# Kernel optimization log

Hardware: AMD Instinct MI355X
Metric: run time of the kernel (lower is better)

## Reference

```python
import jax, jax.numpy as jnp
import numpy as np

M_ZEROS = 15
ZETA_WEIGHT = 0.4
SIGMA = 0.1
# First 15 imaginary parts of nontrivial Riemann zeta zeros (get_zeta_zeros(15))
ZETA_ZEROS = np.array([
    14.134725, 21.022040, 25.010858, 30.424876, 32.935062,
    37.586178, 40.918719, 43.327073, 48.005151, 49.773832,
    52.970321, 56.446248, 59.347044, 60.831779, 65.112544,
], dtype=np.float32)

B, T, I, H = 64, 1024, 512, 512


def setup_inputs() -> dict:
    key = jax.random.key(0)
    k = jax.random.split(key, 6)
    s_ih = 1.0 / np.sqrt(I)
    s_hh = 1.0 / np.sqrt(H)
    x = jax.random.normal(k[0], (B, T, I), dtype=jnp.float32)
    W_ih = jax.random.normal(k[1], (4 * H, I), dtype=jnp.float32) * s_ih
    W_hh = jax.random.normal(k[2], (4 * H, H), dtype=jnp.float32) * s_hh
    b_ih = jax.random.normal(k[3], (4 * H,), dtype=jnp.float32) * s_hh
    b_hh = jax.random.normal(k[4], (4 * H,), dtype=jnp.float32) * s_hh
    gammas = jnp.asarray(ZETA_ZEROS)
    phi_init = np.exp(-SIGMA * np.abs(ZETA_ZEROS))
    log_phi = jnp.asarray(np.log(np.exp(phi_init) - 1 + 1e-6).astype(np.float32))
    return {"x": x, "W_ih": W_ih, "W_hh": W_hh, "b_ih": b_ih,
            "b_hh": b_hh, "log_phi": log_phi, "gammas": gammas}


def _zeta_lstm(x, W_ih, W_hh, b_ih, b_hh, log_phi, gammas):
    Bq, Tq, _ = x.shape
    Hq = W_hh.shape[1]
    # Precompute scalar zeta mixing weight per timestep: w_t = sum(phi * cos(g*t)) / M
    phi = jax.nn.softplus(log_phi)                     # [M]
    t_idx = jnp.arange(Tq, dtype=jnp.float32)          # [T]
    cos_mat = jnp.cos(t_idx[:, None] * gammas[None, :])  # [T, M]
    w_ts = (cos_mat @ phi) / M_ZEROS                   # [T]
    # Hoist the input projection out of the scan: [B,T,4H]
    x_proj = jnp.einsum('bti,gi->btg', x, W_ih) + b_ih + b_hh

    def step(carry, inp):
        h, c = carry
        xp_t, w_t = inp
        gates = xp_t + h @ W_hh.T                      # [B, 4H]
        ig, fg, gg, og = jnp.split(gates, 4, axis=-1)
        c_new = jax.nn.sigmoid(fg) * c + jax.nn.sigmoid(ig) * jnp.tanh(gg)
        h_new = jax.nn.sigmoid(og) * jnp.tanh(c_new)
        # zeta memory uses the PREVIOUS h
        h_out = h_new + ZETA_WEIGHT * (w_t * h)
        return (h_out, c_new), h_out

    h0 = jnp.zeros((Bq, Hq), dtype=x.dtype)
    c0 = jnp.zeros((Bq, Hq), dtype=x.dtype)
    xs = (jnp.transpose(x_proj, (1, 0, 2)), w_ts)
    (h_f, c_f), outs = jax.lax.scan(step, (h0, c0), xs)
    outputs = jnp.transpose(outs, (1, 0, 2))           # [B, T, H]
    return outputs, h_f[None, :, :], c_f[None, :, :]


def reference(x, W_ih, W_hh, b_ih, b_hh, log_phi, gammas):
    return _zeta_lstm(x, W_ih, W_hh, b_ih, b_hh, log_phi, gammas)
```

## Files before the change

### kernel.cpp

```cpp
#include <hip/hip_runtime.h>

#define BDIM 64
#define TDIM 1024
#define IDIM 512
#define HDIM 512
#define G4   2048
#define DSLAB 8
#define SLAB_ELEMS (BDIM * HDIM)
#define GROUP_ELEMS (16 * HDIM)

typedef unsigned short u16;
typedef unsigned int u32;
typedef unsigned long long u64;
typedef __attribute__((ext_vector_type(8))) short short8;
typedef __attribute__((ext_vector_type(4))) float f32x4;

__device__ __forceinline__ u16 f2bf(float f) {
    union { float f; unsigned u; } v; v.f = f;
    unsigned u = v.u;
    return (u16)((u + 0x7fffu + ((u >> 16) & 1u)) >> 16);
}
__device__ __forceinline__ float bf2f(u16 h) {
    union { unsigned u; float f; } v; v.u = ((unsigned)h) << 16;
    return v.f;
}
__device__ __forceinline__ float fsig(float x) {
    float e = __builtin_amdgcn_exp2f(x * -1.4426950408889634f);
    return __builtin_amdgcn_rcpf(1.0f + e);
}
__device__ __forceinline__ float ftanh(float x) {
    float e = __builtin_amdgcn_exp2f(x * -2.8853900817779268f);
    return 2.0f * __builtin_amdgcn_rcpf(1.0f + e) - 1.0f;
}

__global__ void prep_kernel(const float* __restrict__ Whh,
                            const float* __restrict__ bih,
                            const float* __restrict__ bhh,
                            const float* __restrict__ log_phi,
                            const float* __restrict__ gammas,
                            u16* __restrict__ whh_bf,
                            float* __restrict__ bias,
                            float* __restrict__ wfull,
                            u32* __restrict__ hbuf32) {
    int idx = blockIdx.x * 256 + threadIdx.x;
    if (idx < G4 * HDIM) whh_bf[idx] = f2bf(Whh[idx]);
    if (idx < G4) bias[idx] = bih[idx] + bhh[idx];
    if (idx < DSLAB * (SLAB_ELEMS / 2))
        hbuf32[idx] = (idx < (SLAB_ELEMS / 2)) ? 0u : 0xffffffffu;
    if (idx < TDIM) {
        float acc = 0.0f;
        #pragma unroll
        for (int m = 0; m < 15; ++m) {
            float lp = log_phi[m];
            float sp = (lp > 15.0f) ? lp : log1pf(expf(lp));
            acc += sp * cosf((float)idx * gammas[m]);
        }
        wfull[idx] = 0.4f * acc / 15.0f;
    }
}

__global__ __launch_bounds__(256) void xproj_gemm(
        const float* __restrict__ X, const float* __restrict__ Wih,
        const float* __restrict__ bias, u16* __restrict__ xproj) {
    const int tid  = threadIdx.x;
    const int m0   = blockIdx.x * 128;
    const int n0   = blockIdx.y * 128;
    const int lane = tid & 63, w = tid >> 6;
    const int l16  = lane & 15, lhi = lane >> 4;
    const int wr   = w >> 1, wc = w & 1;

    __shared__ u16 As[128 * 64];
    __shared__ u16 Bs[128 * 64];

    f32x4 acc[4][4];
    #pragma unroll
    for (int i = 0; i < 4; ++i)
        #pragma unroll
        for (int j = 0; j < 4; ++j) acc[i][j] = (f32x4){0.f, 0.f, 0.f, 0.f};

    for (int kt = 0; kt < 8; ++kt) {
        const int k0 = kt * 64;
        __syncthreads();
        #pragma unroll
        for (int p = 0; p < 4; ++p) {
            int g = p * 256 + tid;
            int row = g >> 3, oct = g & 7;
            const float* src = X + (size_t)(m0 + row) * IDIM + k0 + oct * 8;
            float4 v0 = *(const float4*)src;
            float4 v1 = *(const float4*)(src + 4);
            short8 u;
            u[0] = (short)f2bf(v0.x); u[1] = (short)f2bf(v0.y);
            u[2] = (short)f2bf(v0.z); u[3] = (short)f2bf(v0.w);
            u[4] = (short)f2bf(v1.x); u[5] = (short)f2bf(v1.y);
            u[6] = (short)f2bf(v1.z); u[7] = (short)f2bf(v1.w);
            int so = (oct ^ (row & 7)) * 8;
            *(short8*)&As[row * 64 + so] = u;
        }
        #pragma unroll
        for (int p = 0; p < 4; ++p) {
            int g = p * 256 + tid;
            int row = g >> 3, oct = g & 7;
            const float* src = Wih + (size_t)(n0 + row) * IDIM + k0 + oct * 8;
            float4 v0 = *(const float4*)src;
            float4 v1 = *(const float4*)(src + 4);
            short8 u;
            u[0] = (short)f2bf(v0.x); u[1] = (short)f2bf(v0.y);
            u[2] = (short)f2bf(v0.z); u[3] = (short)f2bf(v0.w);
            u[4] = (short)f2bf(v1.x); u[5] = (short)f2bf(v1.y);
            u[6] = (short)f2bf(v1.z); u[7] = (short)f2bf(v1.w);
            int so = (oct ^ (row & 7)) * 8;
            *(short8*)&Bs[row * 64 + so] = u;
        }
        __syncthreads();
        #pragma unroll
        for (int ks = 0; ks < 2; ++ks) {
            short8 a[4], b[4];
            #pragma unroll
            for (int ai = 0; ai < 4; ++ai) {
                int row = 64 * wr + 16 * ai + l16;
                int oct = (4 * ks + lhi) ^ (row & 7);
                a[ai] = *(const short8*)&As[row * 64 + oct * 8];
            }
            #pragma unroll
            for (int bi = 0; bi < 4; ++bi) {
                int row = 64 * wc + 16 * bi + l16;
                int oct = (4 * ks + lhi) ^ (row & 7);
                b[bi] = *(const short8*)&Bs[row * 64 + oct * 8];
            }
            #pragma unroll
            for (int ai = 0; ai < 4; ++ai)
                #pragma unroll
                for (int bi = 0; bi < 4; ++bi)
                    acc[ai][bi] = __builtin_amdgcn_mfma_f32_16x16x32_bf16(
                        a[ai], b[bi], acc[ai][bi], 0, 0, 0);
        }
    }
    float bv[4];
    #pragma unroll
    for (int bi = 0; bi < 4; ++bi) bv[bi] = bias[n0 + 64 * wc + 16 * bi + l16];
    #pragma unroll
    for (int ai = 0; ai < 4; ++ai) {
        int grow_base = m0 + 64 * wr + 16 * ai + 4 * lhi;
        #pragma unroll
        for (int bi = 0; bi < 4; ++bi) {
            int gcol = n0 + 64 * wc + 16 * bi + l16;
            #pragma unroll
            for (int r = 0; r < 4; ++r) {
                int grow = grow_base + r;
                int b = grow >> 10;
                int t = grow & 1023;
                xproj[((size_t)t * BDIM + b) * G4 + gcol] =
                    f2bf(acc[ai][bi][r] + bv[bi]);
            }
        }
    }
}

__global__ __launch_bounds__(256, 1) void scan_kernel(
        const u16* __restrict__ whh_bf, const float* __restrict__ wfull,
        const u16* __restrict__ xproj, u16* __restrict__ hbuf,
        float* __restrict__ out) {
    const int tid = threadIdx.x;
    const int blk = blockIdx.x;
    const int bg  = blk >> 4;
    const int cgp = blk & 15;
    const int b0  = bg * 16;
    const int c0  = cgp * 32;
    const int lane = tid & 63, w = tid >> 6;
    const int l16 = lane & 15, lhi = lane >> 4;

    __shared__ u16  hfrag[16 * 64 * 8];
    __shared__ float gates[16 * 128];
    __shared__ float wt_s[TDIM];

    for (int i = tid; i < TDIM; i += 256) wt_s[i] = wfull[i];

    short8 Bf0[16], Bf1[16];
    #pragma unroll
    for (int ks = 0; ks < 16; ++ks) {
        int row0 = w * HDIM + c0 + l16;
        int row1 = w * HDIM + c0 + 16 + l16;
        Bf0[ks] = *(const short8*)&whh_bf[(size_t)row0 * HDIM + ks * 32 + lhi * 8];
        Bf1[ks] = *(const short8*)&whh_bf[(size_t)row1 * HDIM + ks * 32 + lhi * 8];
    }

    const int eb = tid >> 4;
    const int j0 = 2 * (tid & 15);
    const int gcol = c0 + j0;
    const int ln_e = eb + 16 * (j0 >> 3);
    const size_t eidx = ((size_t)cgp * 64 + ln_e) * 8 + (j0 & 7);
    float creg0 = 0.f, creg1 = 0.f;
    float hp0 = 0.f, hp1 = 0.f;

    u32 xq0, xq1, xq2, xq3;
    {
        const u16* xb = xproj + (size_t)(b0 + eb) * G4 + gcol;
        xq0 = *(const u32*)(xb + 0 * HDIM);
        xq1 = *(const u32*)(xb + 1 * HDIM);
        xq2 = *(const u32*)(xb + 2 * HDIM);
        xq3 = *(const u32*)(xb + 3 * HDIM);
    }
    __syncthreads();

    for (int t = 0; t < TDIM; ++t) {
        const u16* hsrc = hbuf + (size_t)(t & 7) * SLAB_ELEMS
                               + (size_t)bg * GROUP_ELEMS;

        union F { u64 q[2]; short8 s; } A4[4];
        for (;;) {
            u32 bad = 0;
            #pragma unroll
            for (int i = 0; i < 4; ++i) {
                const int ks = 4 * w + i;
                const u64* p = (const u64*)(hsrc + ks * 512 + lane * 8);
                u64 lo = __hip_atomic_load(p, __ATOMIC_RELAXED, __HIP_MEMORY_SCOPE_AGENT);
                u64 hi = __hip_atomic_load(p + 1, __ATOMIC_RELAXED, __HIP_MEMORY_SCOPE_AGENT);
                A4[i].q[0] = lo; A4[i].q[1] = hi;
                bad |= ((u32)lo == 0xffffffffu) | ((u32)(lo >> 32) == 0xffffffffu) |
                       ((u32)hi == 0xffffffffu) | ((u32)(hi >> 32) == 0xffffffffu);
            }
            if (!__any((int)bad)) break;
        }

        if (t > 0) {
            *(float2*)(out + ((size_t)(b0 + eb) * TDIM + (t - 1)) * HDIM + gcol) =
                make_float2(hp0, hp1);
        }
        u32 nx0 = 0, nx1 = 0, nx2 = 0, nx3 = 0;
        if (t + 1 < TDIM) {
            const u16* xb = xproj + (size_t)(t + 1) * BDIM * G4 +
                            (size_t)(b0 + eb) * G4 + gcol;
            nx0 = *(const u32*)(xb + 0 * HDIM);
            nx1 = *(const u32*)(xb + 1 * HDIM);
            nx2 = *(const u32*)(xb + 2 * HDIM);
            nx3 = *(const u32*)(xb + 3 * HDIM);
        }

        #pragma unroll
        for (int i = 0; i < 4; ++i) {
            const int ks = 4 * w + i;
            *(short8*)&hfrag[(ks * 64 + lane) * 8] = A4[i].s;
        }
        __syncthreads();
        if (t > 0) {
            __hip_atomic_store(
                (u32*)(hbuf + (size_t)((t - 1) & 7) * SLAB_ELEMS +
                       (size_t)bg * GROUP_ELEMS + eidx), 0xffffffffu,
                __ATOMIC_RELAXED, __HIP_MEMORY_SCOPE_AGENT);
        }

        f32x4 acc0a = {0.f, 0.f, 0.f, 0.f}, acc0b = {0.f, 0.f, 0.f, 0.f};
        f32x4 acc1a = {0.f, 0.f, 0.f, 0.f}, acc1b = {0.f, 0.f, 0.f, 0.f};
        #pragma unroll
        for (int ks = 0; ks < 8; ++ks) {
            short8 a  = *(const short8*)&hfrag[(ks * 64 + lane) * 8];
            short8 a2 = *(const short8*)&hfrag[((ks + 8) * 64 + lane) * 8];
            acc0a = __builtin_amdgcn_mfma_f32_16x16x32_bf16(a,  Bf0[ks],     acc0a, 0, 0, 0);
            acc1a = __builtin_amdgcn_mfma_f32_16x16x32_bf16(a,  Bf1[ks],     acc1a, 0, 0, 0);
            acc0b = __builtin_amdgcn_mfma_f32_16x16x32_bf16(a2, Bf0[ks + 8], acc0b, 0, 0, 0);
            acc1b = __builtin_amdgcn_mfma_f32_16x16x32_bf16(a2, Bf1[ks + 8], acc1b, 0, 0, 0);
        }
        f32x4 acc0 = acc0a + acc0b;
        f32x4 acc1 = acc1a + acc1b;
        #pragma unroll
        for (int r = 0; r < 4; ++r) {
            gates[(4 * lhi + r) * 128 + w * 32 + l16]      = acc0[r];
            gates[(4 * lhi + r) * 128 + w * 32 + 16 + l16] = acc1[r];
        }
        __syncthreads();

        const float wt = wt_s[t];
        float x0 = bf2f((u16)(xq0 & 0xffff)), x1 = bf2f((u16)(xq0 >> 16));
        float f0 = bf2f((u16)(xq1 & 0xffff)), f1 = bf2f((u16)(xq1 >> 16));
        float g0 = bf2f((u16)(xq2 & 0xffff)), g1 = bf2f((u16)(xq2 >> 16));
        float o0 = bf2f((u16)(xq3 & 0xffff)), o1 = bf2f((u16)(xq3 >> 16));

        float gi0 = gates[eb * 128 + 0 * 32 + j0]     + x0;
        float gi1 = gates[eb * 128 + 0 * 32 + j0 + 1] + x1;
        float gf0 = gates[eb * 128 + 1 * 32 + j0]     + f0;
        float gf1 = gates[eb * 128 + 1 * 32 + j0 + 1] + f1;
        float gg0 = gates[eb * 128 + 2 * 32 + j0]     + g0;
        float gg1 = gates[eb * 128 + 2 * 32 + j0 + 1] + g1;
        float go0 = gates[eb * 128 + 3 * 32 + j0]     + o0;
        float go1 = gates[eb * 128 + 3 * 32 + j0 + 1] + o1;

        float cn0 = fsig(gf0) * creg0 + fsig(gi0) * ftanh(gg0);
        float cn1 = fsig(gf1) * creg1 + fsig(gi1) * ftanh(gg1);
        float ho0 = fsig(go0) * ftanh(cn0) + wt * hp0;
        float ho1 = fsig(go1) * ftanh(cn1) + wt * hp1;
        creg0 = cn0; creg1 = cn1;
        hp0 = ho0; hp1 = ho1;

        u32 hw = (u32)f2bf(ho0) | ((u32)f2bf(ho1) << 16);
        __hip_atomic_store(
            (u32*)(hbuf + (size_t)((t + 1) & 7) * SLAB_ELEMS +
                   (size_t)bg * GROUP_ELEMS + eidx), hw,
            __ATOMIC_RELAXED, __HIP_MEMORY_SCOPE_AGENT);

        xq0 = nx0; xq1 = nx1; xq2 = nx2; xq3 = nx3;
    }

    *(float2*)(out + ((size_t)(b0 + eb) * TDIM + (TDIM - 1)) * HDIM + gcol) =
        make_float2(hp0, hp1);
    size_t base = (size_t)BDIM * TDIM * HDIM;
    *(float2*)(out + base + (size_t)(b0 + eb) * HDIM + gcol) =
        make_float2(hp0, hp1);
    *(float2*)(out + base + (size_t)BDIM * HDIM + (size_t)(b0 + eb) * HDIM + gcol) =
        make_float2(creg0, creg1);
}

extern "C" void kernel_launch(void* const* d_in, const int* in_sizes, int n_in,
                              void* d_out, int out_size, void* d_ws, size_t ws_size,
                              hipStream_t stream) {
    const float* x       = (const float*)d_in[0];
    const float* Wih     = (const float*)d_in[1];
    const float* Whh     = (const float*)d_in[2];
    const float* bih     = (const float*)d_in[3];
    const float* bhh     = (const float*)d_in[4];
    const float* log_phi = (const float*)d_in[5];
    const float* gammas  = (const float*)d_in[6];
    float* out = (float*)d_out;

    char* ws = (char*)d_ws;
    u16*   whh_bf = (u16*)(ws);
    float* bias   = (float*)(ws + (2u << 20));
    float* wfull  = (float*)(ws + (2u << 20) + 8192);
    u16*   hbuf   = (u16*)(ws + (3u << 20));
    u16*   xproj  = (u16*)(ws + (4u << 20));

    prep_kernel<<<dim3(4096), dim3(256), 0, stream>>>(
        Whh, bih, bhh, log_phi, gammas, whh_bf, bias, wfull, (u32*)hbuf);

    xproj_gemm<<<dim3(512, 16), dim3(256), 0, stream>>>(x, Wih, bias, xproj);

    scan_kernel<<<dim3(64), dim3(256), 0, stream>>>(
        whh_bf, wfull, xproj, hbuf, out);
}
```

Baseline: 2.673 ms.

## Fuse input-projection GEMM with recurrent scan using poisoned xproj flags

Merges the input-projection GEMM and the sequential LSTM scan into one launch. The first 64 blocks run the scan while the remaining blocks compute xproj tiles ordered by time chunk. The scan spins on per-element 0xffff poison values, written into xproj by the prep kernel, until the data it needs is ready. This is meant to overlap the GEMM with the latency-bound recurrence, at the cost of a 256 MB poison fill in prep, atomic loads on xproj, and a deadlock risk if scan blocks occupy CUs before producer blocks are scheduled. A real bf16 value of 0xffff (a NaN pattern) would also spin forever.

```diff
diff --git a/kernel.cpp b/kernel.cpp
--- a/kernel.cpp
+++ b/kernel.cpp
@@ -8,12 +8,14 @@
 #define DSLAB 8
 #define SLAB_ELEMS (BDIM * HDIM)
 #define GROUP_ELEMS (16 * HDIM)
+#define XPROJ_U32 ((size_t)BDIM * TDIM * G4 / 2)
 
 typedef unsigned short u16;
 typedef unsigned int u32;
 typedef unsigned long long u64;
 typedef __attribute__((ext_vector_type(8))) short short8;
 typedef __attribute__((ext_vector_type(4))) float f32x4;
+typedef __attribute__((ext_vector_type(4))) unsigned int u32x4;
 
 __device__ __forceinline__ u16 f2bf(float f) {
     union { float f; unsigned u; } v; v.f = f;
@@ -31,6 +33,9 @@
 __device__ __forceinline__ float ftanh(float x) {
     float e = __builtin_amdgcn_exp2f(x * -2.8853900817779268f);
     return 2.0f * __builtin_amdgcn_rcpf(1.0f + e) - 1.0f;
+}
+__device__ __forceinline__ u32 pois(u32 w) {
+    return ((w & 0xffffu) == 0xffffu) | ((w >> 16) == 0xffffu);
 }
 
 __global__ void prep_kernel(const float* __restrict__ Whh,
@@ -41,9 +46,10 @@
                             u16* __restrict__ whh_bf,
                             float* __restrict__ bias,
                             float* __restrict__ wfull,
-                            u32* __restrict__ hbuf32) {
-    int idx = blockIdx.x * 256 + threadIdx.x;
-    if (idx < G4 * HDIM) whh_bf[idx] = f2bf(Whh[idx]);
+                            u32* __restrict__ hbuf32,
+                            u32* __restrict__ xproj32) {
+    size_t idx = (size_t)blockIdx.x * 256 + threadIdx.x;
+    if (idx < (size_t)G4 * HDIM) whh_bf[idx] = f2bf(Whh[idx]);
     if (idx < G4) bias[idx] = bih[idx] + bhh[idx];
     if (idx < DSLAB * (SLAB_ELEMS / 2))
         hbuf32[idx] = (idx < (SLAB_ELEMS / 2)) ? 0u : 0xffffffffu;
@@ -57,256 +63,273 @@
         }
         wfull[idx] = 0.4f * acc / 15.0f;
     }
-}
-
-__global__ __launch_bounds__(256) void xproj_gemm(
+    if (idx < XPROJ_U32 / 4) {
+        u32x4 p = {0xffffffffu, 0xffffffffu, 0xffffffffu, 0xffffffffu};
+        *(u32x4*)(xproj32 + idx * 4) = p;
+    }
+}
+
+__global__ __launch_bounds__(256, 1) void fused_kernel(
+        const u16* __restrict__ whh_bf, const float* __restrict__ wfull,
         const float* __restrict__ X, const float* __restrict__ Wih,
-        const float* __restrict__ bias, u16* __restrict__ xproj) {
-    const int tid  = threadIdx.x;
-    const int m0   = blockIdx.x * 128;
-    const int n0   = blockIdx.y * 128;
-    const int lane = tid & 63, w = tid >> 6;
-    const int l16  = lane & 15, lhi = lane >> 4;
-    const int wr   = w >> 1, wc = w & 1;
-
-    __shared__ u16 As[128 * 64];
-    __shared__ u16 Bs[128 * 64];
-
-    f32x4 acc[4][4];
-    #pragma unroll
-    for (int i = 0; i < 4; ++i)
-        #pragma unroll
-        for (int j = 0; j < 4; ++j) acc[i][j] = (f32x4){0.f, 0.f, 0.f, 0.f};
-
-    for (int kt = 0; kt < 8; ++kt) {
-        const int k0 = kt * 64;
-        __syncthreads();
-        #pragma unroll
-        for (int p = 0; p < 4; ++p) {
-            int g = p * 256 + tid;
-            int row = g >> 3, oct = g & 7;
-            const float* src = X + (size_t)(m0 + row) * IDIM + k0 + oct * 8;
-            float4 v0 = *(const float4*)src;
-            float4 v1 = *(const float4*)(src + 4);
-            short8 u;
-            u[0] = (short)f2bf(v0.x); u[1] = (short)f2bf(v0.y);
-            u[2] = (short)f2bf(v0.z); u[3] = (short)f2bf(v0.w);
-            u[4] = (short)f2bf(v1.x); u[5] = (short)f2bf(v1.y);
-            u[6] = (short)f2bf(v1.z); u[7] = (short)f2bf(v1.w);
-            int so = (oct ^ (row & 7)) * 8;
-            *(short8*)&As[row * 64 + so] = u;
-        }
-        #pragma unroll
-        for (int p = 0; p < 4; ++p) {
-            int g = p * 256 + tid;
-            int row = g >> 3, oct = g & 7;
-            const float* src = Wih + (size_t)(n0 + row) * IDIM + k0 + oct * 8;
-            float4 v0 = *(const float4*)src;
-            float4 v1 = *(const float4*)(src + 4);
-            short8 u;
-            u[0] = (short)f2bf(v0.x); u[1] = (short)f2bf(v0.y);
-            u[2] = (short)f2bf(v0.z); u[3] = (short)f2bf(v0.w);
-            u[4] = (short)f2bf(v1.x); u[5] = (short)f2bf(v1.y);
-            u[6] = (short)f2bf(v1.z); u[7] = (short)f2bf(v1.w);
-            int so = (oct ^ (row & 7)) * 8;
-            *(short8*)&Bs[row * 64 + so] = u;
-        }
-        __syncthreads();
-        #pragma unroll
-        for (int ks = 0; ks < 2; ++ks) {
-            short8 a[4], b[4];
-            #pragma unroll
-            for (int ai = 0; ai < 4; ++ai) {
-                int row = 64 * wr + 16 * ai + l16;
-                int oct = (4 * ks + lhi) ^ (row & 7);
-                a[ai] = *(const short8*)&As[row * 64 + oct * 8];
-            }
-            #pragma unroll
-            for (int bi = 0; bi < 4; ++bi) {
-                int row = 64 * wc + 16 * bi + l16;
-                int oct = (4 * ks + lhi) ^ (row & 7);
-                b[bi] = *(const short8*)&Bs[row * 64 + oct * 8];
-            }
-            #pragma unroll
-            for (int ai = 0; ai < 4; ++ai)
-                #pragma unroll
-                for (int bi = 0; bi < 4; ++bi)
-                    acc[ai][bi] = __builtin_amdgcn_mfma_f32_16x16x32_bf16(
-                        a[ai], b[bi], acc[ai][bi], 0, 0, 0);
-        }
-    }
-    float bv[4];
-    #pragma unroll
-    for (int bi = 0; bi < 4; ++bi) bv[bi] = bias[n0 + 64 * wc + 16 * bi + l16];
-    #pragma unroll
-    for (int ai = 0; ai < 4; ++ai) {
-        int grow_base = m0 + 64 * wr + 16 * ai + 4 * lhi;
-        #pragma unroll
-        for (int bi = 0; bi < 4; ++bi) {
-            int gcol = n0 + 64 * wc + 16 * bi + l16;
-            #pragma unroll
-            for (int r = 0; r < 4; ++r) {
-                int grow = grow_base + r;
-                int b = grow >> 10;
-                int t = grow & 1023;
-                xproj[((size_t)t * BDIM + b) * G4 + gcol] =
-                    f2bf(acc[ai][bi][r] + bv[bi]);
-            }
-        }
-    }
-}
-
-__global__ __launch_bounds__(256, 1) void scan_kernel(
-        const u16* __restrict__ whh_bf, const float* __restrict__ wfull,
-        const u16* __restrict__ xproj, u16* __restrict__ hbuf,
-        float* __restrict__ out) {
+        const float* __restrict__ bias, u16* __restrict__ xproj,
+        u16* __restrict__ hbuf, float* __restrict__ out) {
     const int tid = threadIdx.x;
-    const int blk = blockIdx.x;
-    const int bg  = blk >> 4;
-    const int cgp = blk & 15;
-    const int b0  = bg * 16;
-    const int c0  = cgp * 32;
     const int lane = tid & 63, w = tid >> 6;
     const int l16 = lane & 15, lhi = lane >> 4;
 
-    __shared__ u16  hfrag[16 * 64 * 8];
-    __shared__ float gates[16 * 128];
-    __shared__ float wt_s[TDIM];
-
-    for (int i = tid; i < TDIM; i += 256) wt_s[i] = wfull[i];
-
-    short8 Bf0[16], Bf1[16];
-    #pragma unroll
-    for (int ks = 0; ks < 16; ++ks) {
-        int row0 = w * HDIM + c0 + l16;
-        int row1 = w * HDIM + c0 + 16 + l16;
-        Bf0[ks] = *(const short8*)&whh_bf[(size_t)row0 * HDIM + ks * 32 + lhi * 8];
-        Bf1[ks] = *(const short8*)&whh_bf[(size_t)row1 * HDIM + ks * 32 + lhi * 8];
-    }
-
-    const int eb = tid >> 4;
-    const int j0 = 2 * (tid & 15);
-    const int gcol = c0 + j0;
-    const int ln_e = eb + 16 * (j0 >> 3);
-    const size_t eidx = ((size_t)cgp * 64 + ln_e) * 8 + (j0 & 7);
-    float creg0 = 0.f, creg1 = 0.f;
-    float hp0 = 0.f, hp1 = 0.f;
-
-    u32 xq0, xq1, xq2, xq3;
-    {
-        const u16* xb = xproj + (size_t)(b0 + eb) * G4 + gcol;
-        xq0 = *(const u32*)(xb + 0 * HDIM);
-        xq1 = *(const u32*)(xb + 1 * HDIM);
-        xq2 = *(const u32*)(xb + 2 * HDIM);
-        xq3 = *(const u32*)(xb + 3 * HDIM);
-    }
-    __syncthreads();
-
-    for (int t = 0; t < TDIM; ++t) {
-        const u16* hsrc = hbuf + (size_t)(t & 7) * SLAB_ELEMS
-                               + (size_t)bg * GROUP_ELEMS;
-
-        union F { u64 q[2]; short8 s; } A4[4];
-        for (;;) {
-            u32 bad = 0;
+    __shared__ char smem[32768];
+
+    if (blockIdx.x < 64) {
+        u16*   hfrag = (u16*)smem;
+        float* gates = (float*)(smem + 16384);
+        float* wt_s  = (float*)(smem + 24576);
+
+        const int blk = blockIdx.x;
+        const int bg  = blk >> 4;
+        const int cgp = blk & 15;
+        const int b0  = bg * 16;
+        const int c0  = cgp * 32;
+
+        for (int i = tid; i < TDIM; i += 256) wt_s[i] = wfull[i];
+
+        short8 Bf0[16], Bf1[16];
+        #pragma unroll
+        for (int ks = 0; ks < 16; ++ks) {
+            int row0 = w * HDIM + c0 + l16;
+            int row1 = w * HDIM + c0 + 16 + l16;
+            Bf0[ks] = *(const short8*)&whh_bf[(size_t)row0 * HDIM + ks * 32 + lhi * 8];
+            Bf1[ks] = *(const short8*)&whh_bf[(size_t)row1 * HDIM + ks * 32 + lhi * 8];
+        }
+
+        const int eb = tid >> 4;
+        const int j0 = 2 * (tid & 15);
+        const int gcol = c0 + j0;
+        const int ln_e = eb + 16 * (j0 >> 3);
+        const size_t eidx = ((size_t)cgp * 64 + ln_e) * 8 + (j0 & 7);
+        float creg0 = 0.f, creg1 = 0.f;
+        float hp0 = 0.f, hp1 = 0.f;
+
+        u32 xq0, xq1, xq2, xq3;
+        {
+            const u16* xb = xproj + (size_t)(b0 + eb) * G4 + gcol;
+            xq0 = __hip_atomic_load((const u32*)(xb + 0 * HDIM), __ATOMIC_RELAXED, __HIP_MEMORY_SCOPE_AGENT);
+            xq1 = __hip_atomic_load((const u32*)(xb + 1 * HDIM), __ATOMIC_RELAXED, __HIP_MEMORY_SCOPE_AGENT);
+            xq2 = __hip_atomic_load((const u32*)(xb + 2 * HDIM), __ATOMIC_RELAXED, __HIP_MEMORY_SCOPE_AGENT);
+            xq3 = __hip_atomic_load((const u32*)(xb + 3 * HDIM), __ATOMIC_RELAXED, __HIP_MEMORY_SCOPE_AGENT);
+        }
+        __syncthreads();
+
+        for (int t = 0; t < TDIM; ++t) {
+            const u16* hsrc = hbuf + (size_t)(t & 7) * SLAB_ELEMS
+                                   + (size_t)bg * GROUP_ELEMS;
+
+            union F { u64 q[2]; short8 s; } A4[4];
+            for (;;) {
+                u32 bad = 0;
+                #pragma unroll
+                for (int i = 0; i < 4; ++i) {
+                    const int ks = 4 * w + i;
+                    const u64* p = (const u64*)(hsrc + ks * 512 + lane * 8);
+                    u64 lo = __hip_atomic_load(p, __ATOMIC_RELAXED, __HIP_MEMORY_SCOPE_AGENT);
+                    u64 hi = __hip_atomic_load(p + 1, __ATOMIC_RELAXED, __HIP_MEMORY_SCOPE_AGENT);
+                    A4[i].q[0] = lo; A4[i].q[1] = hi;
+                    bad |= ((u32)lo == 0xffffffffu) | ((u32)(lo >> 32) == 0xffffffffu) |
+                           ((u32)hi == 0xffffffffu) | ((u32)(hi >> 32) == 0xffffffffu);
+                }
+                if (!__any((int)bad)) break;
+            }
+
+            while (pois(xq0) | pois(xq1) | pois(xq2) | pois(xq3)) {
+                const u16* xb = xproj + (size_t)t * BDIM * G4 +
+                                (size_t)(b0 + eb) * G4 + gcol;
+                xq0 = __hip_atomic_load((const u32*)(xb + 0 * HDIM), __ATOMIC_RELAXED, __HIP_MEMORY_SCOPE_AGENT);
+                xq1 = __hip_atomic_load((const u32*)(xb + 1 * HDIM), __ATOMIC_RELAXED, __HIP_MEMORY_SCOPE_AGENT);
+                xq2 = __hip_atomic_load((const u32*)(xb + 2 * HDIM), __ATOMIC_RELAXED, __HIP_MEMORY_SCOPE_AGENT);
+                xq3 = __hip_atomic_load((const u32*)(xb + 3 * HDIM), __ATOMIC_RELAXED, __HIP_MEMORY_SCOPE_AGENT);
+            }
+
+            if (t > 0) {
+                *(float2*)(out + ((size_t)(b0 + eb) * TDIM + (t - 1)) * HDIM + gcol) =
+                    make_float2(hp0, hp1);
+            }
+            u32 nx0 = 0, nx1 = 0, nx2 = 0, nx3 = 0;
+            if (t + 1 < TDIM) {
+                const u16* xb = xproj + (size_t)(t + 1) * BDIM * G4 +
+                                (size_t)(b0 + eb) * G4 + gcol;
+                nx0 = __hip_atomic_load((const u32*)(xb + 0 * HDIM), __ATOMIC_RELAXED, __HIP_MEMORY_SCOPE_AGENT);
+                nx1 = __hip_atomic_load((const u32*)(xb + 1 * HDIM), __ATOMIC_RELAXED, __HIP_MEMORY_SCOPE_AGENT);
+                nx2 = __hip_atomic_load((const u32*)(xb + 2 * HDIM), __ATOMIC_RELAXED, __HIP_MEMORY_SCOPE_AGENT);
+                nx3 = __hip_atomic_load((const u32*)(xb + 3 * HDIM), __ATOMIC_RELAXED, __HIP_MEMORY_SCOPE_AGENT);
+            }
+
             #pragma unroll
             for (int i = 0; i < 4; ++i) {
                 const int ks = 4 * w + i;
-                const u64* p = (const u64*)(hsrc + ks * 512 + lane * 8);
-                u64 lo = __hip_atomic_load(p, __ATOMIC_RELAXED, __HIP_MEMORY_SCOPE_AGENT);
-                u64 hi = __hip_atomic_load(p + 1, __ATOMIC_RELAXED, __HIP_MEMORY_SCOPE_AGENT);
-                A4[i].q[0] = lo; A4[i].q[1] = hi;
-                bad |= ((u32)lo == 0xffffffffu) | ((u32)(lo >> 32) == 0xffffffffu) |
-                       ((u32)hi == 0xffffffffu) | ((u32)(hi >> 32) == 0xffffffffu);
-            }
-            if (!__any((int)bad)) break;
-        }
-
-        if (t > 0) {
-            *(float2*)(out + ((size_t)(b0 + eb) * TDIM + (t - 1)) * HDIM + gcol) =
-                make_float2(hp0, hp1);
-        }
-        u32 nx0 = 0, nx1 = 0, nx2 = 0, nx3 = 0;
-        if (t + 1 < TDIM) {
-            const u16* xb = xproj + (size_t)(t + 1) * BDIM * G4 +
-                            (size_t)(b0 + eb) * G4 + gcol;
-            nx0 = *(const u32*)(xb + 0 * HDIM);
-            nx1 = *(const u32*)(xb + 1 * HDIM);
-            nx2 = *(const u32*)(xb + 2 * HDIM);
-            nx3 = *(const u32*)(xb + 3 * HDIM);
-        }
-
-        #pragma unroll
-        for (int i = 0; i < 4; ++i) {
-            const int ks = 4 * w + i;
-            *(short8*)&hfrag[(ks * 64 + lane) * 8] = A4[i].s;
-        }
-        __syncthreads();
-        if (t > 0) {
+                *(short8*)&hfrag[(ks * 64 + lane) * 8] = A4[i].s;
+            }
+            __syncthreads();
+            if (t > 0) {
+                __hip_atomic_store(
+                    (u32*)(hbuf + (size_t)((t - 1) & 7) * SLAB_ELEMS +
+                           (size_t)bg * GROUP_ELEMS + eidx), 0xffffffffu,
+                    __ATOMIC_RELAXED, __HIP_MEMORY_SCOPE_AGENT);
+            }
+
+            f32x4 acc0a = {0.f, 0.f, 0.f, 0.f}, acc0b = {0.f, 0.f, 0.f, 0.f};
+            f32x4 acc1a = {0.f, 0.f, 0.f, 0.f}, acc1b = {0.f, 0.f, 0.f, 0.f};
+            #pragma unroll
+            for (int ks = 0; ks < 8; ++ks) {
+                short8 a  = *(const short8*)&hfrag[(ks * 64 + lane) * 8];
+                short8 a2 = *(const short8*)&hfrag[((ks + 8) * 64 + lane) * 8];
+                acc0a = __builtin_amdgcn_mfma_f32_16x16x32_bf16(a,  Bf0[ks],     acc0a, 0, 0, 0);
+                acc1a = __builtin_amdgcn_mfma_f32_16x16x32_bf16(a,  Bf1[ks],     acc1a, 0, 0, 0);
+                acc0b = __builtin_amdgcn_mfma_f32_16x16x32_bf16(a2, Bf0[ks + 8], acc0b, 0, 0, 0);
+                acc1b = __builtin_amdgcn_mfma_f32_16x16x32_bf16(a2, Bf1[ks + 8], acc1b, 0, 0, 0);
+            }
+            f32x4 acc0 = acc0a + acc0b;
+            f32x4 acc1 = acc1a + acc1b;
+            #pragma unroll
+            for (int r = 0; r < 4; ++r) {
+                gates[(4 * lhi + r) * 128 + w * 32 + l16]      = acc0[r];
+                gates[(4 * lhi + r) * 128 + w * 32 + 16 + l16] = acc1[r];
+            }
+            __syncthreads();
+
+            const float wt = wt_s[t];
+            float x0 = bf2f((u16)(xq0 & 0xffff)), x1 = bf2f((u16)(xq0 >> 16));
+            float f0 = bf2f((u16)(xq1 & 0xffff)), f1 = bf2f((u16)(xq1 >> 16));
+            float g0 = bf2f((u16)(xq2 & 0xffff)), g1 = bf2f((u16)(xq2 >> 16));
+            float o0 = bf2f((u16)(xq3 & 0xffff)), o1 = bf2f((u16)(xq3 >> 16));
+
+            float gi0 = gates[eb * 128 + 0 * 32 + j0]     + x0;
+            float gi1 = gates[eb * 128 + 0 * 32 + j0 + 1] + x1;
+            float gf0 = gates[eb * 128 + 1 * 32 + j0]     + f0;
+            float gf1 = gates[eb * 128 + 1 * 32 + j0 + 1] + f1;
+            float gg0 = gates[eb * 128 + 2 * 32 + j0]     + g0;
+            float gg1 = gates[eb * 128 + 2 * 32 + j0 + 1] + g1;
+            float go0 = gates[eb * 128 + 3 * 32 + j0]     + o0;
+            float go1 = gates[eb * 128 + 3 * 32 + j0 + 1] + o1;
+
+            float cn0 = fsig(gf0) * creg0 + fsig(gi0) * ftanh(gg0);
+            float cn1 = fsig(gf1) * creg1 + fsig(gi1) * ftanh(gg1);
+            float ho0 = fsig(go0) * ftanh(cn0) + wt * hp0;
+            float ho1 = fsig(go1) * ftanh(cn1) + wt * hp1;
+            creg0 = cn0; creg1 = cn1;
+            hp0 = ho0; hp1 = ho1;
+
+            u32 hw = (u32)f2bf(ho0) | ((u32)f2bf(ho1) << 16);
             __hip_atomic_store(
-                (u32*)(hbuf + (size_t)((t - 1) & 7) * SLAB_ELEMS +
-                       (size_t)bg * GROUP_ELEMS + eidx), 0xffffffffu,
+                (u32*)(hbuf + (size_t)((t + 1) & 7) * SLAB_ELEMS +
+                       (size_t)bg * GROUP_ELEMS + eidx), hw,
                 __ATOMIC_RELAXED, __HIP_MEMORY_SCOPE_AGENT);
-        }
-
-        f32x4 acc0a = {0.f, 0.f, 0.f, 0.f}, acc0b = {0.f, 0.f, 0.f, 0.f};
-        f32x4 acc1a = {0.f, 0.f, 0.f, 0.f}, acc1b = {0.f, 0.f, 0.f, 0.f};
-        #pragma unroll
-        for (int ks = 0; ks < 8; ++ks) {
-            short8 a  = *(const short8*)&hfrag[(ks * 64 + lane) * 8];
-            short8 a2 = *(const short8*)&hfrag[((ks + 8) * 64 + lane) * 8];
-            acc0a = __builtin_amdgcn_mfma_f32_16x16x32_bf16(a,  Bf0[ks],     acc0a, 0, 0, 0);
-            acc1a = __builtin_amdgcn_mfma_f32_16x16x32_bf16(a,  Bf1[ks],     acc1a, 0, 0, 0);
-            acc0b = __builtin_amdgcn_mfma_f32_16x16x32_bf16(a2, Bf0[ks + 8], acc0b, 0, 0, 0);
-            acc1b = __builtin_amdgcn_mfma_f32_16x16x32_bf16(a2, Bf1[ks + 8], acc1b, 0, 0, 0);
-        }
-        f32x4 acc0 = acc0a + acc0b;
-        f32x4 acc1 = acc1a + acc1b;
-        #pragma unroll
-        for (int r = 0; r < 4; ++r) {
-            gates[(4 * lhi + r) * 128 + w * 32 + l16]      = acc0[r];
-            gates[(4 * lhi + r) * 128 + w * 32 + 16 + l16] = acc1[r];
-        }
-        __syncthreads();
-
-        const float wt = wt_s[t];
-        float x0 = bf2f((u16)(xq0 & 0xffff)), x1 = bf2f((u16)(xq0 >> 16));
-        float f0 = bf2f((u16)(xq1 & 0xffff)), f1 = bf2f((u16)(xq1 >> 16));
-        float g0 = bf2f((u16)(xq2 & 0xffff)), g1 = bf2f((u16)(xq2 >> 16));
-        float o0 = bf2f((u16)(xq3 & 0xffff)), o1 = bf2f((u16)(xq3 >> 16));
-
-        float gi0 = gates[eb * 128 + 0 * 32 + j0]     + x0;
-        float gi1 = gates[eb * 128 + 0 * 32 + j0 + 1] + x1;
-        float gf0 = gates[eb * 128 + 1 * 32 + j0]     + f0;
-        float gf1 = gates[eb * 128 + 1 * 32 + j0 + 1] + f1;
-        float gg0 = gates[eb * 128 + 2 * 32 + j0]     + g0;
-        float gg1 = gates[eb * 128 + 2 * 32 + j0 + 1] + g1;
-        float go0 = gates[eb * 128 + 3 * 32 + j0]     + o0;
-        float go1 = gates[eb * 128 + 3 * 32 + j0 + 1] + o1;
-
-        float cn0 = fsig(gf0) * creg0 + fsig(gi0) * ftanh(gg0);
-        float cn1 = fsig(gf1) * creg1 + fsig(gi1) * ftanh(gg1);
-        float ho0 = fsig(go0) * ftanh(cn0) + wt * hp0;
-        float ho1 = fsig(go1) * ftanh(cn1) + wt * hp1;
-        creg0 = cn0; creg1 = cn1;
-        hp0 = ho0; hp1 = ho1;
-
-        u32 hw = (u32)f2bf(ho0) | ((u32)f2bf(ho1) << 16);
-        __hip_atomic_store(
-            (u32*)(hbuf + (size_t)((t + 1) & 7) * SLAB_ELEMS +
-                   (size_t)bg * GROUP_ELEMS + eidx), hw,
-            __ATOMIC_RELAXED, __HIP_MEMORY_SCOPE_AGENT);
-
-        xq0 = nx0; xq1 = nx1; xq2 = nx2; xq3 = nx3;
+
+            xq0 = nx0; xq1 = nx1; xq2 = nx2; xq3 = nx3;
+        }
+
+        *(float2*)(out + ((size_t)(b0 + eb) * TDIM + (TDIM - 1)) * HDIM + gcol) =
+            make_float2(hp0, hp1);
+        size_t base = (size_t)BDIM * TDIM * HDIM;
+        *(float2*)(out + base + (size_t)(b0 + eb) * HDIM + gcol) =
+            make_float2(hp0, hp1);
+        *(float2*)(out + base + (size_t)BDIM * HDIM + (size_t)(b0 + eb) * HDIM + gcol) =
+            make_float2(creg0, creg1);
+
+    } else {
+        u16* As = (u16*)smem;
+        u16* Bs = (u16*)(smem + 16384);
+
+        const int lin    = blockIdx.x - 64;
+        const int ycol   = lin & 15;
+        const int gx     = lin >> 4;
+        const int tchunk = gx >> 6;
+        const int bb     = gx & 63;
+        const int m0     = bb * 1024 + tchunk * 128;
+        const int n0     = ycol * 128;
+        const int wr     = w >> 1, wc = w & 1;
+
+        f32x4 acc[4][4];
+        #pragma unroll
+        for (int i = 0; i < 4; ++i)
+            #pragma unroll
+            for (int j = 0; j < 4; ++j) acc[i][j] = (f32x4){0.f, 0.f, 0.f, 0.f};
+
+        for (int kt = 0; kt < 8; ++kt) {
+            const int k0 = kt * 64;
+            __syncthreads();
+            #pragma unroll
+            for (int p = 0; p < 4; ++p) {
+                int g = p * 256 + tid;
+                int row = g >> 3, oct = g & 7;
+                const float* src = X + (size_t)(m0 + row) * IDIM + k0 + oct * 8;
+                float4 v0 = *(const float4*)src;
+                float4 v1 = *(const float4*)(src + 4);
+                short8 u;
+                u[0] = (short)f2bf(v0.x); u[1] = (short)f2bf(v0.y);
+                u[2] = (short)f2bf(v0.z); u[3] = (short)f2bf(v0.w);
+                u[4] = (short)f2bf(v1.x); u[5] = (short)f2bf(v1.y);
+                u[6] = (short)f2bf(v1.z); u[7] = (short)f2bf(v1.w);
+                *(short8*)&As[row * 64 + ((oct ^ (row & 7)) * 8)] = u;
+            }
+            #pragma unroll
+            for (int p = 0; p < 4; ++p) {
+                int g = p * 256 + tid;
+                int row = g >> 3, oct = g & 7;
+                const float* src = Wih + (size_t)(n0 + row) * IDIM + k0 + oct * 8;
+                float4 v0 = *(const float4*)src;
+                float4 v1 = *(const float4*)(src + 4);
+                short8 u;
+                u[0] = (short)f2bf(v0.x); u[1] = (short)f2bf(v0.y);
+                u[2] = (short)f2bf(v0.z); u[3] = (short)f2bf(v0.w);
+                u[4] = (short)f2bf(v1.x); u[5] = (short)f2bf(v1.y);
+                u[6] = (short)f2bf(v1.z); u[7] = (short)f2bf(v1.w);
+                *(short8*)&Bs[row * 64 + ((oct ^ (row & 7)) * 8)] = u;
+            }
+            __syncthreads();
+            #pragma unroll
+            for (int ks = 0; ks < 2; ++ks) {
+                short8 a[4], b[4];
+                #pragma unroll
+                for (int ai = 0; ai < 4; ++ai) {
+                    int row = 64 * wr + 16 * ai + l16;
+                    int oct = (4 * ks + lhi) ^ (row & 7);
+                    a[ai] = *(const short8*)&As[row * 64 + oct * 8];
+                }
+                #pragma unroll
+                for (int bi = 0; bi < 4; ++bi) {
+                    int row = 64 * wc + 16 * bi + l16;
+                    int oct = (4 * ks + lhi) ^ (row & 7);
+                    b[bi] = *(const short8*)&Bs[row * 64 + oct * 8];
+                }
+                #pragma unroll
+                for (int ai = 0; ai < 4; ++ai)
+                    #pragma unroll
+                    for (int bi = 0; bi < 4; ++bi)
+                        acc[ai][bi] = __builtin_amdgcn_mfma_f32_16x16x32_bf16(
+                            a[ai], b[bi], acc[ai][bi], 0, 0, 0);
+            }
+        }
+        float bv[4];
+        #pragma unroll
+        for (int bi = 0; bi < 4; ++bi) bv[bi] = bias[n0 + 64 * wc + 16 * bi + l16];
+        #pragma unroll
+        for (int ai = 0; ai < 4; ++ai) {
+            int grow_base = m0 + 64 * wr + 16 * ai + 4 * lhi;
+            #pragma unroll
+            for (int bi = 0; bi < 4; ++bi) {
+                int gcol2 = n0 + 64 * wc + 16 * bi + l16;
+                #pragma unroll
+                for (int r = 0; r < 4; ++r) {
+                    int grow = grow_base + r;
+                    int b = grow >> 10;
+                    int t = grow & 1023;
+                    xproj[((size_t)t * BDIM + b) * G4 + gcol2] =
+                        f2bf(acc[ai][bi][r] + bv[bi]);
+                }
+            }
+        }
+        __threadfence();
     }
-
-    *(float2*)(out + ((size_t)(b0 + eb) * TDIM + (TDIM - 1)) * HDIM + gcol) =
-        make_float2(hp0, hp1);
-    size_t base = (size_t)BDIM * TDIM * HDIM;
-    *(float2*)(out + base + (size_t)(b0 + eb) * HDIM + gcol) =
-        make_float2(hp0, hp1);
-    *(float2*)(out + base + (size_t)BDIM * HDIM + (size_t)(b0 + eb) * HDIM + gcol) =
-        make_float2(creg0, creg1);
 }
 
 extern "C" void kernel_launch(void* const* d_in, const int* in_sizes, int n_in,
@@ -328,11 +351,10 @@
     u16*   hbuf   = (u16*)(ws + (3u << 20));
     u16*   xproj  = (u16*)(ws + (4u << 20));
 
-    prep_kernel<<<dim3(4096), dim3(256), 0, stream>>>(
-        Whh, bih, bhh, log_phi, gammas, whh_bf, bias, wfull, (u32*)hbuf);
-
-    xproj_gemm<<<dim3(512, 16), dim3(256), 0, stream>>>(x, Wih, bias, xproj);
-
-    scan_kernel<<<dim3(64), dim3(256), 0, stream>>>(
-        whh_bf, wfull, xproj, hbuf, out);
-}
+    prep_kernel<<<dim3(65536), dim3(256), 0, stream>>>(
+        Whh, bih, bhh, log_phi, gammas, whh_bf, bias, wfull,
+        (u32*)hbuf, (u32*)xproj);
+
+    fused_kernel<<<dim3(64 + 8192), dim3(256), 0, stream>>>(
+        whh_bf, wfull, x, Wih, bias, xproj, hbuf, out);
+}
```

Measured after the change: 4.064 ms. +52.1%, slower.
